# Kernel optimization log

Hardware: AMD Instinct MI355X
Metric: run time of the kernel (lower is better)

Reference implementation:

```python
import jax, jax.numpy as jnp
import numpy as np

D_MODEL = 1024
NUM_HEADS = 16
HEAD_DIM = D_MODEL // NUM_HEADS


def setup_inputs() -> dict:
    key = jax.random.key(0)
    ks = jax.random.split(key, 11)
    B, S = 2, 2048
    inp = {
        "query": jax.random.normal(ks[0], (B, S, D_MODEL), jnp.float32),
        "key": jax.random.normal(ks[1], (B, S, D_MODEL), jnp.float32),
        "value": jax.random.normal(ks[2], (B, S, D_MODEL), jnp.float32),
        "mask": 1,
        "w_q": jax.random.normal(ks[3], (D_MODEL, D_MODEL), jnp.float32) / np.sqrt(D_MODEL),
        "b_q": jax.random.normal(ks[4], (D_MODEL,), jnp.float32) * 0.02,
        "w_k": jax.random.normal(ks[5], (D_MODEL, D_MODEL), jnp.float32) / np.sqrt(D_MODEL),
        "b_k": jax.random.normal(ks[6], (D_MODEL,), jnp.float32) * 0.02,
        "w_v": jax.random.normal(ks[7], (D_MODEL, D_MODEL), jnp.float32) / np.sqrt(D_MODEL),
        "b_v": jax.random.normal(ks[8], (D_MODEL,), jnp.float32) * 0.02,
        "w_o": jax.random.normal(ks[9], (D_MODEL, D_MODEL), jnp.float32) / np.sqrt(D_MODEL),
        "b_o": jax.random.normal(ks[10], (D_MODEL,), jnp.float32) * 0.02,
    }
    return inp


def reference(query, key, value, mask, w_q, b_q, w_k, b_k, w_v, b_v, w_o, b_o):
    B, S, _ = query.shape
    H, Dh = NUM_HEADS, HEAD_DIM
    # projections (torch Linear: x @ W.T + b; here w_* stored as [in, out])
    q = (query @ w_q + b_q).reshape(B, S, H, Dh).transpose(0, 2, 1, 3)  # [B,H,S,Dh]
    k = (key @ w_k + b_k).reshape(B, S, H, Dh).transpose(0, 2, 1, 3)
    v = (value @ w_v + b_v).reshape(B, S, H, Dh).transpose(0, 2, 1, 3)
    scale = 1.0 / jnp.sqrt(jnp.asarray(Dh, q.dtype))
    scores = jnp.einsum("bhqd,bhkd->bhqk", q, k) * scale  # [B,H,S,S]
    if mask:
        causal = jnp.tril(jnp.ones((S, S), dtype=bool))
        scores = jnp.where(causal, scores, jnp.asarray(-1e9, scores.dtype))
    attn = jax.nn.softmax(scores, axis=-1)
    x = jnp.einsum("bhqk,bhkd->bhqd", attn, v)  # [B,H,S,Dh]
    x = x.transpose(0, 2, 1, 3).reshape(B, S, H * Dh)
    return x @ w_o + b_o
```

## Files before the change

kernel.cpp:

```cpp
#include <hip/hip_runtime.h>
#include <hip/hip_bf16.h>

using bf16 = __hip_bfloat16;

typedef __attribute__((ext_vector_type(4))) short short4v;
typedef __attribute__((ext_vector_type(8))) short short8v;
typedef __attribute__((ext_vector_type(4))) float f32x4;

static constexpr int D  = 1024;
static constexpr int H  = 16;
static constexpr int DH = 64;
static constexpr int B  = 2;
static constexpr int S  = 2048;
static constexpr int M  = B * S;
static constexpr size_t MD = (size_t)M * D;
static constexpr size_t WSZ = (size_t)D * D;

#define QS_CONST 0.18033688011112042f

__device__ __forceinline__ unsigned short f2b(float f) {
    union { float f; unsigned u; } v; v.f = f;
    return (unsigned short)((v.u + 0x7FFFu + ((v.u >> 16) & 1u)) >> 16);
}
__device__ __forceinline__ unsigned pkbf(float a, float b) {
    float2 t; t.x = a; t.y = b;
    __hip_bfloat162 h = __float22bfloat162_rn(t);
    union { __hip_bfloat162 h; unsigned u; } cv; cv.h = h;
    return cv.u;
}
__device__ __forceinline__ short8v pack8(short4v a, short4v b) {
    short8v r;
    r[0]=a[0]; r[1]=a[1]; r[2]=a[2]; r[3]=a[3];
    r[4]=b[0]; r[5]=b[1]; r[6]=b[2]; r[7]=b[3];
    return r;
}
__device__ __forceinline__ short8v ld_frag(const short* rowp, int lg) {
    short4v a = *reinterpret_cast<const short4v*>(rowp + 4*lg);
    short4v b = *reinterpret_cast<const short4v*>(rowp + 16 + 4*lg);
    return pack8(a, b);
}

__device__ __forceinline__ void gl_lds16(const void* g, void* l) {
    __builtin_amdgcn_global_load_lds(
        (const __attribute__((address_space(1))) unsigned int*)g,
        (__attribute__((address_space(3))) unsigned int*)l, 16, 0, 0);
}

__global__ __launch_bounds__(256) void cvt_x_kernel(
    const float* __restrict__ x0, const float* __restrict__ x1,
    const float* __restrict__ x2,
    unsigned short* __restrict__ y0, unsigned short* __restrict__ y1,
    unsigned short* __restrict__ y2)
{
    const float* X = blockIdx.z==0 ? x0 : blockIdx.z==1 ? x1 : x2;
    unsigned short* Y = blockIdx.z==0 ? y0 : blockIdx.z==1 ? y1 : y2;
    const size_t base = (size_t)blockIdx.x * 256 + threadIdx.x;
    const size_t stride = (size_t)1024 * 256;
#pragma unroll
    for (int j = 0; j < 4; ++j) {
        const size_t i = base + (size_t)j * stride;
        float4 f = reinterpret_cast<const float4*>(X)[i];
        uint2 p; p.x = pkbf(f.x, f.y); p.y = pkbf(f.z, f.w);
        reinterpret_cast<uint2*>(Y)[i] = p;
    }
}

__global__ __launch_bounds__(256) void cvt_w_kernel(
    const float* __restrict__ w0, const float* __restrict__ w1,
    const float* __restrict__ w2, const float* __restrict__ w3,
    unsigned short* __restrict__ t0, unsigned short* __restrict__ t1,
    unsigned short* __restrict__ t2, unsigned short* __restrict__ t3)
{
    __shared__ float tile[32][33];
    const float* W = blockIdx.z==0 ? w0 : blockIdx.z==1 ? w1 : blockIdx.z==2 ? w2 : w3;
    unsigned short* T = blockIdx.z==0 ? t0 : blockIdx.z==1 ? t1 : blockIdx.z==2 ? t2 : t3;
    const int k0 = blockIdx.x*32, n0 = blockIdx.y*32;
    const int t = threadIdx.x, r = t>>3, c4 = (t&7)*4;
    float4 v = *reinterpret_cast<const float4*>(&W[(size_t)(k0+r)*D + n0 + c4]);
    tile[r][c4+0]=v.x; tile[r][c4+1]=v.y; tile[r][c4+2]=v.z; tile[r][c4+3]=v.w;
    __syncthreads();
    uint2 p;
    p.x = pkbf(tile[c4+0][r], tile[c4+1][r]);
    p.y = pkbf(tile[c4+2][r], tile[c4+3][r]);
    *reinterpret_cast<uint2*>(T + (size_t)(n0+r)*D + k0 + c4) = p;
}

#define GEMM_CORE_LDS(XPTR, WPTR)                                              \
    __shared__ short As[2][128*32];                                            \
    __shared__ short Bs[2][128*32];                                            \
    const int tid = threadIdx.x;                                               \
    const int wid = tid>>6, lane = tid&63;                                     \
    const int wr = wid>>1, wc = wid&1;                                         \
    const int lg = lane>>4, lr = lane&15;                                      \
    const int qw = (lane&3) ^ ((lane>>3)&3);        \
    const int qr = lg ^ ((lr>>1)&3);                \
    f32x4 acc[4][4];                                                           \
    _Pragma("unroll")                                                          \
    for (int i=0;i<4;i++)                                                      \
        _Pragma("unroll")                                                      \
        for (int j=0;j<4;j++) acc[i][j] = f32x4{0.f,0.f,0.f,0.f};              \
    const int srow = (lane>>2);                                                \
    auto stage = [&](int buf, int k0) {                                        \
        _Pragma("unroll")                                                      \
        for (int c=0;c<2;c++) {                                                \
            const int r0 = 32*wid + 16*c;                                      \
            const int r  = r0 + srow;                                          \
            gl_lds16(XPTR + (size_t)(m0+r)*1024 + k0 + qw*8, &As[buf][r0*32]); \
            gl_lds16(WPTR + (size_t)(n0+r)*1024 + k0 + qw*8, &Bs[buf][r0*32]); \
        }                                                                      \
    };                                                                         \
    stage(0, 0);                                                               \
    int cur = 0;                                                               \
    for (int k0 = 0; k0 < 1024; k0 += 32) {                                    \
        __syncthreads();                     \
        if (k0 + 32 < 1024) stage(cur^1, k0 + 32);                             \
        short8v af[4], bfr[4];                                                 \
        _Pragma("unroll")                                                      \
        for (int i=0;i<4;i++) {                                                \
            const int R = wr*64 + i*16 + lr;                                   \
            af[i] = *reinterpret_cast<const short8v*>(&As[cur][R*32 + qr*8]);  \
        }                                                                      \
        _Pragma("unroll")                                                      \
        for (int j=0;j<4;j++) {                                                \
            const int R = wc*64 + j*16 + lr;                                   \
            bfr[j] = *reinterpret_cast<const short8v*>(&Bs[cur][R*32 + qr*8]); \
        }                                                                      \
        __builtin_amdgcn_s_setprio(1);                                         \
        _Pragma("unroll")                                                      \
        for (int i=0;i<4;i++)                                                  \
            _Pragma("unroll")                                                  \
            for (int j=0;j<4;j++)                                              \
                acc[i][j] = __builtin_amdgcn_mfma_f32_16x16x32_bf16(           \
                    af[i], bfr[j], acc[i][j], 0,0,0);                          \
        __builtin_amdgcn_s_setprio(0);                                         \
        cur ^= 1;                                                              \
    }

__global__ __launch_bounds__(256) void gemm_qkv_lds(
    const unsigned short* __restrict__ Xq, const unsigned short* __restrict__ Xk,
    const unsigned short* __restrict__ Xv, const unsigned short* __restrict__ WtBase,
    const float* __restrict__ bq, const float* __restrict__ bk,
    const float* __restrict__ bv, unsigned short* __restrict__ qkBase,
    unsigned short* __restrict__ va)
{
    const int z = blockIdx.z;
    const unsigned short* X = z==0 ? Xq : z==1 ? Xk : Xv;
    const unsigned short* Wt = WtBase + (size_t)z * WSZ;
    const float* bias = z==0 ? bq : z==1 ? bk : bv;
    const int m0 = blockIdx.x*128, n0 = blockIdx.y*128;

    GEMM_CORE_LDS(X, Wt)

#pragma unroll
    for (int i=0;i<4;i++) {
#pragma unroll
        for (int j=0;j<4;j++) {
            const int n = n0 + wc*64 + j*16 + lr;
            const float bv2 = bias[n];
#pragma unroll
            for (int r=0;r<4;r++) {
                const int m = m0 + wr*64 + i*16 + lg*4 + r;
                float v = acc[i][j][r] + bv2;
                const int bb=m>>11, ss=m&2047, hh=n>>6, dh=n&63;
                if (z == 0) {
                    v *= QS_CONST;
                    qkBase[(((size_t)(bb*H+hh))*S + ss)*DH + dh] = f2b(v);
                } else if (z == 1) {
                    (qkBase + MD)[(((size_t)(bb*H+hh))*S + ss)*DH + dh] = f2b(v);
                } else {
                    va[(((size_t)(bb*H+hh))*DH + dh)*S + ss] = f2b(v);
                }
            }
        }
    }
}

template<int OUTBF>
__global__ __launch_bounds__(256) void gemm_out_lds(
    const unsigned short* __restrict__ Xc, const unsigned short* __restrict__ Wt,
    const float* __restrict__ bias, void* __restrict__ Y)
{
    const int m0 = blockIdx.x*128, n0 = blockIdx.y*128;

    GEMM_CORE_LDS(Xc, Wt)

#pragma unroll
    for (int i=0;i<4;i++) {
#pragma unroll
        for (int j=0;j<4;j++) {
            const int n = n0 + wc*64 + j*16 + lr;
            const float bv = bias[n];
#pragma unroll
            for (int r=0;r<4;r++) {
                const int m = m0 + wr*64 + i*16 + lg*4 + r;
                const float v = acc[i][j][r] + bv;
                if (OUTBF) ((unsigned short*)Y)[(size_t)m*D + n] = f2b(v);
                else       ((float*)Y)[(size_t)m*D + n] = v;
            }
        }
    }
}

__global__ __launch_bounds__(256) void attn_mfma(
    const unsigned short* __restrict__ Qa,
    const unsigned short* __restrict__ Ka,
    const unsigned short* __restrict__ Va,
    unsigned short* __restrict__ Ctx)
{
    __shared__ short Ks[2][64][72];
    __shared__ short Vs[2][64][72];
    short (*Ob)[72] = Ks[0];

    const int tid = threadIdx.x;
    const int i   = blockIdx.x;
    const int xcd = i & 7;
    const int o   = i >> 3;
    const int bh  = (xcd << 2) + (o >> 5);
    const int qt  = ((o >> 5) & 1) ? (o & 31) : 31 - (o & 31);
    const int bb = bh>>4, hh = bh&15;
    const int q0 = qt*64;
    const int wid = tid>>6, lane = tid&63;
    const int lg = lane>>4, lr = lane&15;
    const size_t qkbase = (size_t)bh*S*DH;
    const size_t vbase  = (size_t)bh*DH*S;

    const int qrow = q0 + wid*16 + lr;
    short8v qf[2];
    {
        const unsigned short* qp = Qa + qkbase + (size_t)qrow*DH;
#pragma unroll
        for (int c=0;c<2;c++) {
            short4v a = *reinterpret_cast<const short4v*>(qp + 32*c + 4*lg);
            short4v b = *reinterpret_cast<const short4v*>(qp + 32*c + 16 + 4*lg);
            qf[c] = pack8(a, b);
        }
    }

    float lsum = 0.f;
    f32x4 oacc[4];
#pragma unroll
    for (int dt=0;dt<4;dt++) oacc[dt] = f32x4{0.f,0.f,0.f,0.f};

    const int sr = tid>>2;
    const int sc = (tid&3)*16;

    uint4 kg0, kg1, vg0, vg1;
    auto load_kv = [&](int j0) {
        const unsigned short* kp = Ka + qkbase + (size_t)(j0+sr)*DH + sc;
        kg0 = *reinterpret_cast<const uint4*>(kp);
        kg1 = *reinterpret_cast<const uint4*>(kp + 8);
        const unsigned short* vp = Va + vbase + (size_t)sr*S + j0 + sc;
        vg0 = *reinterpret_cast<const uint4*>(vp);
        vg1 = *reinterpret_cast<const uint4*>(vp + 8);
    };
    auto store_kv = [&](int buf) {
        *reinterpret_cast<uint4*>(&Ks[buf][sr][sc])   = kg0;
        *reinterpret_cast<uint4*>(&Ks[buf][sr][sc+8]) = kg1;
        *reinterpret_cast<uint4*>(&Vs[buf][sr][sc])   = vg0;
        *reinterpret_cast<uint4*>(&Vs[buf][sr][sc+8]) = vg1;
    };

    const int NT = qt + 1;
    load_kv(0);
    store_kv(0);

    for (int t = 0; t < NT; ++t) {
        const int j0 = t*64;
        const int cur = t & 1;
        if (t + 1 < NT) load_kv(j0 + 64);
        __syncthreads();

        __builtin_amdgcn_s_setprio(1);
        f32x4 st[4];
#pragma unroll
        for (int jt=0;jt<4;jt++) {
            f32x4 s = f32x4{0.f,0.f,0.f,0.f};
#pragma unroll
            for (int c=0;c<2;c++) {
                short8v kf = ld_frag(&Ks[cur][jt*16 + lr][32*c], lg);
                s = __builtin_amdgcn_mfma_f32_16x16x32_bf16(kf, qf[c], s, 0,0,0);
            }
            st[jt] = s;
        }
        __builtin_amdgcn_s_setprio(0);

        float p[16];
        if (t == NT-1) {
#pragma unroll
            for (int jt=0;jt<4;jt++)
#pragma unroll
                for (int r=0;r<4;r++) {
                    const int j = j0 + jt*16 + lg*4 + r;
                    p[jt*4+r] = (j <= qrow) ? st[jt][r] : -1e30f;
                }
        } else {
#pragma unroll
            for (int jt=0;jt<4;jt++)
#pragma unroll
                for (int r=0;r<4;r++) p[jt*4+r] = st[jt][r];
        }
#pragma unroll
        for (int e=0;e<16;e++) { p[e] = exp2f(p[e]); lsum += p[e]; }

        uint4 u0, u1;
        u0.x = pkbf(p[0],p[1]);   u0.y = pkbf(p[2],p[3]);
        u0.z = pkbf(p[4],p[5]);   u0.w = pkbf(p[6],p[7]);
        u1.x = pkbf(p[8],p[9]);   u1.y = pkbf(p[10],p[11]);
        u1.z = pkbf(p[12],p[13]); u1.w = pkbf(p[14],p[15]);
        short8v pf0, pf1;
        *reinterpret_cast<uint4*>(&pf0) = u0;
        *reinterpret_cast<uint4*>(&pf1) = u1;

        __builtin_amdgcn_s_setprio(1);
#pragma unroll
        for (int dt=0;dt<4;dt++) {
            short8v vf0 = ld_frag(&Vs[cur][dt*16 + lr][0],  lg);
            short8v vf1 = ld_frag(&Vs[cur][dt*16 + lr][32], lg);
            oacc[dt] = __builtin_amdgcn_mfma_f32_16x16x32_bf16(vf0, pf0, oacc[dt], 0,0,0);
            oacc[dt] = __builtin_amdgcn_mfma_f32_16x16x32_bf16(vf1, pf1, oacc[dt], 0,0,0);
        }
        __builtin_amdgcn_s_setprio(0);

        if (t + 1 < NT) store_kv(cur ^ 1);
    }

    lsum += __shfl_xor(lsum, 16);
    lsum += __shfl_xor(lsum, 32);
    __syncthreads();
    const float inv = 1.f / lsum;
#pragma unroll
    for (int dt=0;dt<4;dt++) {
        uint2 w;
        w.x = pkbf(oacc[dt][0]*inv, oacc[dt][1]*inv);
        w.y = pkbf(oacc[dt][2]*inv, oacc[dt][3]*inv);
        *reinterpret_cast<uint2*>(&Ob[wid*16 + lr][dt*16 + lg*4]) = w;
    }
    __syncthreads();
    const int orow = tid>>2, oc = (tid&3)*16;
    uint4 o1 = *reinterpret_cast<const uint4*>(&Ob[orow][oc]);
    uint4 o2 = *reinterpret_cast<const uint4*>(&Ob[orow][oc+8]);
    unsigned short* dst = Ctx + ((size_t)bb*S + q0 + orow)*D + hh*DH + oc;
    *reinterpret_cast<uint4*>(dst)     = o1;
    *reinterpret_cast<uint4*>(dst + 8) = o2;
}

__global__ __launch_bounds__(256) void gemm_qkv_f32(
    const float* __restrict__ Xq, const float* __restrict__ Xk,
    const float* __restrict__ Xv, const unsigned short* __restrict__ WtBase,
    const float* __restrict__ bq, const float* __restrict__ bk,
    const float* __restrict__ bv, unsigned short* __restrict__ qkBase,
    unsigned short* __restrict__ va)
{
    constexpr int K = 1024;
    __shared__ short As[128][40];
    __shared__ short Bs[128][40];

    const int z = blockIdx.z;
    const float* X = z==0 ? Xq : z==1 ? Xk : Xv;
    const unsigned short* Wt = WtBase + (size_t)z * WSZ;
    const float* bias = z==0 ? bq : z==1 ? bk : bv;

    const int tid = threadIdx.x;
    const int m0 = blockIdx.x*128, n0 = blockIdx.y*128;
    const int wid = tid>>6, lane = tid&63;
    const int wr = wid>>1, wc = wid&1;
    const int lg = lane>>4, lr = lane&15;

    f32x4 acc[4][4];
#pragma unroll
    for (int i=0;i<4;i++)
#pragma unroll
        for (int j=0;j<4;j++) acc[i][j] = f32x4{0.f,0.f,0.f,0.f};

    const int arow = tid>>1, acol = (tid&1)*16;
    float4 fx0, fx1, fx2, fx3;
    uint4 wa, wb;

    auto load_glb = [&](int k0) {
        const float* Xp = X + (size_t)(m0+arow)*K + k0 + acol;
        fx0 = *reinterpret_cast<const float4*>(Xp+0);
        fx1 = *reinterpret_cast<const float4*>(Xp+4);
        fx2 = *reinterpret_cast<const float4*>(Xp+8);
        fx3 = *reinterpret_cast<const float4*>(Xp+12);
        const unsigned short* Wp = Wt + (size_t)(n0+arow)*K + k0 + acol;
        wa = *reinterpret_cast<const uint4*>(Wp);
        wb = *reinterpret_cast<const uint4*>(Wp + 8);
    };
    auto store_stage = [&]() {
        uint4 p0; p0.x=pkbf(fx0.x,fx0.y); p0.y=pkbf(fx0.z,fx0.w);
                  p0.z=pkbf(fx1.x,fx1.y); p0.w=pkbf(fx1.z,fx1.w);
        uint4 p1; p1.x=pkbf(fx2.x,fx2.y); p1.y=pkbf(fx2.z,fx2.w);
                  p1.z=pkbf(fx3.x,fx3.y); p1.w=pkbf(fx3.z,fx3.w);
        *reinterpret_cast<uint4*>(&As[arow][acol])   = p0;
        *reinterpret_cast<uint4*>(&As[arow][acol+8]) = p1;
        *reinterpret_cast<uint4*>(&Bs[arow][acol])   = wa;
        *reinterpret_cast<uint4*>(&Bs[arow][acol+8]) = wb;
    };

    load_glb(0);
    for (int k0 = 0; k0 < K; k0 += 32) {
        __syncthreads();
        store_stage();
        if (k0 + 32 < K) load_glb(k0 + 32);
        __syncthreads();

        short8v af[4], bfr[4];
#pragma unroll
        for (int i=0;i<4;i++) af[i]  = ld_frag(&As[wr*64 + i*16 + lr][0], lg);
#pragma unroll
        for (int j=0;j<4;j++) bfr[j] = ld_frag(&Bs[wc*64 + j*16 + lr][0], lg);
#pragma unroll
        for (int i=0;i<4;i++)
#pragma unroll
            for (int j=0;j<4;j++)
                acc[i][j] = __builtin_amdgcn_mfma_f32_16x16x32_bf16(af[i], bfr[j], acc[i][j], 0,0,0);
    }

#pragma unroll
    for (int i=0;i<4;i++) {
#pragma unroll
        for (int j=0;j<4;j++) {
            const int n = n0 + wc*64 + j*16 + lr;
            const float bv2 = bias[n];
#pragma unroll
            for (int r=0;r<4;r++) {
                const int m = m0 + wr*64 + i*16 + lg*4 + r;
                float v = acc[i][j][r] + bv2;
                const int bb=m>>11, ss=m&2047, hh=n>>6, dh=n&63;
                if (z == 0) {
                    v *= QS_CONST;
                    qkBase[(((size_t)(bb*H+hh))*S + ss)*DH + dh] = f2b(v);
                } else if (z == 1) {
                    (qkBase + MD)[(((size_t)(bb*H+hh))*S + ss)*DH + dh] = f2b(v);
                } else {
                    va[(((size_t)(bb*H+hh))*DH + dh)*S + ss] = f2b(v);
                }
            }
        }
    }
}

extern "C" void kernel_launch(void* const* d_in, const int* in_sizes, int n_in,
                              void* d_out, int out_size, void* d_ws, size_t ws_size,
                              hipStream_t stream)
{
    const float* query = (const float*)d_in[0];
    const float* key   = (const float*)d_in[1];
    const float* value = (const float*)d_in[2];
    const float* w_q = (const float*)d_in[4];
    const float* b_q = (const float*)d_in[5];
    const float* w_k = (const float*)d_in[6];
    const float* b_k = (const float*)d_in[7];
    const float* w_v = (const float*)d_in[8];
    const float* b_v = (const float*)d_in[9];
    const float* w_o = (const float*)d_in[10];
    const float* b_o = (const float*)d_in[11];

    bool out_bf16 = true;
    {
        size_t ob = 0;
        if (hipMemPtrGetInfo(d_out, &ob) == hipSuccess &&
            ob >= (size_t)out_size * 3 && ob <= (size_t)out_size * 6)
            out_bf16 = false;
    }

    unsigned short* wtq = (unsigned short*)d_ws;
    unsigned short* wtk = wtq + WSZ;
    unsigned short* wtv = wtk + WSZ;
    unsigned short* wto = wtv + WSZ;
    unsigned short* qa  = wto + WSZ;
    unsigned short* ka  = qa  + MD;
    unsigned short* va  = ka  + MD;
    unsigned short* ctx = va  + MD;
    unsigned short* xq  = ctx + MD;
    unsigned short* xk  = xq  + MD;
    unsigned short* xv  = xk  + MD;

    const size_t need_bf16x = (4*WSZ + 7*MD) * sizeof(unsigned short);
    const bool xbf = (ws_size >= need_bf16x);

    cvt_w_kernel<<<dim3(32,32,4), 256, 0, stream>>>(w_q, w_k, w_v, w_o,
                                                    wtq, wtk, wtv, wto);

    if (xbf) {
        cvt_x_kernel<<<dim3(1024,1,3), 256, 0, stream>>>(query, key, value,
                                                         xq, xk, xv);
        gemm_qkv_lds<<<dim3(M/128, D/128, 3), 256, 0, stream>>>(
            xq, xk, xv, wtq, b_q, b_k, b_v, qa, va);
    } else {
        gemm_qkv_f32<<<dim3(M/128, D/128, 3), 256, 0, stream>>>(
            query, key, value, wtq, b_q, b_k, b_v, qa, va);
    }

    attn_mfma<<<dim3((S/64) * B * H), 256, 0, stream>>>(qa, ka, va, ctx);

    if (out_bf16)
        gemm_out_lds<1><<<dim3(M/128, D/128), 256, 0, stream>>>(ctx, wto, b_o, d_out);
    else
        gemm_out_lds<0><<<dim3(M/128, D/128), 256, 0, stream>>>(ctx, wto, b_o, d_out);
}
```

Baseline: 130.1 us.

## Merge conversion kernels and stage attention K/V via direct global-to-LDS loads

Merges the weight-transpose and activation-conversion kernels into one launch, which saves a launch and lets the two run concurrently. The attention kernel now copies K/V tiles with global_load_lds straight into XOR-swizzled unpadded LDS, issued right after the barrier for the next buffer. This replaces the register round-trip and the padding. The fp32 fallback GEMM path is removed, so the code now assumes the workspace is always large enough for the bf16 activations.

```diff
diff --git a/kernel.cpp b/kernel.cpp
--- a/kernel.cpp
+++ b/kernel.cpp
@@ -46,43 +46,43 @@
         (__attribute__((address_space(3))) unsigned int*)l, 16, 0, 0);
 }
 
-__global__ __launch_bounds__(256) void cvt_x_kernel(
+__global__ __launch_bounds__(256) void cvt_all_kernel(
+    const float* __restrict__ w0, const float* __restrict__ w1,
+    const float* __restrict__ w2, const float* __restrict__ w3,
+    unsigned short* __restrict__ t0, unsigned short* __restrict__ t1,
+    unsigned short* __restrict__ t2, unsigned short* __restrict__ t3,
     const float* __restrict__ x0, const float* __restrict__ x1,
     const float* __restrict__ x2,
     unsigned short* __restrict__ y0, unsigned short* __restrict__ y1,
     unsigned short* __restrict__ y2)
 {
-    const float* X = blockIdx.z==0 ? x0 : blockIdx.z==1 ? x1 : x2;
-    unsigned short* Y = blockIdx.z==0 ? y0 : blockIdx.z==1 ? y1 : y2;
-    const size_t base = (size_t)blockIdx.x * 256 + threadIdx.x;
-    const size_t stride = (size_t)1024 * 256;
-#pragma unroll
-    for (int j = 0; j < 4; ++j) {
-        const size_t i = base + (size_t)j * stride;
-        float4 f = reinterpret_cast<const float4*>(X)[i];
-        uint2 p; p.x = pkbf(f.x, f.y); p.y = pkbf(f.z, f.w);
-        reinterpret_cast<uint2*>(Y)[i] = p;
-    }
-}
-
-__global__ __launch_bounds__(256) void cvt_w_kernel(
-    const float* __restrict__ w0, const float* __restrict__ w1,
-    const float* __restrict__ w2, const float* __restrict__ w3,
-    unsigned short* __restrict__ t0, unsigned short* __restrict__ t1,
-    unsigned short* __restrict__ t2, unsigned short* __restrict__ t3)
-{
     __shared__ float tile[32][33];
-    const float* W = blockIdx.z==0 ? w0 : blockIdx.z==1 ? w1 : blockIdx.z==2 ? w2 : w3;
-    unsigned short* T = blockIdx.z==0 ? t0 : blockIdx.z==1 ? t1 : blockIdx.z==2 ? t2 : t3;
-    const int k0 = blockIdx.x*32, n0 = blockIdx.y*32;
-    const int t = threadIdx.x, r = t>>3, c4 = (t&7)*4;
-    float4 v = *reinterpret_cast<const float4*>(&W[(size_t)(k0+r)*D + n0 + c4]);
-    tile[r][c4+0]=v.x; tile[r][c4+1]=v.y; tile[r][c4+2]=v.z; tile[r][c4+3]=v.w;
-    __syncthreads();
-    uint2 p;
-    p.x = pkbf(tile[c4+0][r], tile[c4+1][r]);
-    p.y = pkbf(tile[c4+2][r], tile[c4+3][r]);
-    *reinterpret_cast<uint2*>(T + (size_t)(n0+r)*D + k0 + c4) = p;
+    const int z = blockIdx.z;
+    if (z < 4) {
+        const float* W = z==0 ? w0 : z==1 ? w1 : z==2 ? w2 : w3;
+        unsigned short* T = z==0 ? t0 : z==1 ? t1 : z==2 ? t2 : t3;
+        const int k0 = (blockIdx.x & 31) * 32, n0 = (blockIdx.x >> 5) * 32;
+        const int t = threadIdx.x, r = t>>3, c4 = (t&7)*4;
+        float4 v = *reinterpret_cast<const float4*>(&W[(size_t)(k0+r)*D + n0 + c4]);
+        tile[r][c4+0]=v.x; tile[r][c4+1]=v.y; tile[r][c4+2]=v.z; tile[r][c4+3]=v.w;
+        __syncthreads();
+        uint2 p;
+        p.x = pkbf(tile[c4+0][r], tile[c4+1][r]);
+        p.y = pkbf(tile[c4+2][r], tile[c4+3][r]);
+        *reinterpret_cast<uint2*>(T + (size_t)(n0+r)*D + k0 + c4) = p;
+    } else {
+        const float* X = z==4 ? x0 : z==5 ? x1 : x2;
+        unsigned short* Y = z==4 ? y0 : z==5 ? y1 : y2;
+        const size_t base = (size_t)blockIdx.x * 256 + threadIdx.x;
+        const size_t stride = (size_t)1024 * 256;
+#pragma unroll
+        for (int j = 0; j < 4; ++j) {
+            const size_t i = base + (size_t)j * stride;
+            float4 f = reinterpret_cast<const float4*>(X)[i];
+            uint2 p; p.x = pkbf(f.x, f.y); p.y = pkbf(f.z, f.w);
+            reinterpret_cast<uint2*>(Y)[i] = p;
+        }
+    }
 }
 
 #define GEMM_CORE_LDS(XPTR, WPTR)                                              \
@@ -207,9 +207,9 @@
     const unsigned short* __restrict__ Va,
     unsigned short* __restrict__ Ctx)
 {
-    __shared__ short Ks[2][64][72];
-    __shared__ short Vs[2][64][72];
-    short (*Ob)[72] = Ks[0];
+    __shared__ short Ks[2][64*64];
+    __shared__ short Vs[2][64*64];
+    short (*Ob)[72] = (short(*)[72])Ks;
 
     const int tid = threadIdx.x;
     const int i   = blockIdx.x;
@@ -241,34 +241,36 @@
 #pragma unroll
     for (int dt=0;dt<4;dt++) oacc[dt] = f32x4{0.f,0.f,0.f,0.f};
 
-    const int sr = tid>>2;
-    const int sc = (tid&3)*16;
-
-    uint4 kg0, kg1, vg0, vg1;
-    auto load_kv = [&](int j0) {
-        const unsigned short* kp = Ka + qkbase + (size_t)(j0+sr)*DH + sc;
-        kg0 = *reinterpret_cast<const uint4*>(kp);
-        kg1 = *reinterpret_cast<const uint4*>(kp + 8);
-        const unsigned short* vp = Va + vbase + (size_t)sr*S + j0 + sc;
-        vg0 = *reinterpret_cast<const uint4*>(vp);
-        vg1 = *reinterpret_cast<const uint4*>(vp + 8);
+    const int srsub = lane >> 3;
+    const int scol  = 8 * ((lane & 7) ^ srsub);
+
+    auto stage = [&](int buf, int j0) {
+#pragma unroll
+        for (int c2=0;c2<2;c2++) {
+            const int rb = 16*wid + 8*c2;
+            gl_lds16(Ka + qkbase + (size_t)(j0 + rb + srsub)*DH + scol,
+                     &Ks[buf][rb*64]);
+            gl_lds16(Va + vbase  + (size_t)(rb + srsub)*S + j0 + scol,
+                     &Vs[buf][rb*64]);
+        }
     };
-    auto store_kv = [&](int buf) {
-        *reinterpret_cast<uint4*>(&Ks[buf][sr][sc])   = kg0;
-        *reinterpret_cast<uint4*>(&Ks[buf][sr][sc+8]) = kg1;
-        *reinterpret_cast<uint4*>(&Vs[buf][sr][sc])   = vg0;
-        *reinterpret_cast<uint4*>(&Vs[buf][sr][sc+8]) = vg1;
-    };
+
+    const int r7 = lr & 7;
+    const int l4 = 4*(lg & 1), g0 = lg >> 1;
+    int offA[2], offB[2];
+#pragma unroll
+    for (int c=0;c<2;c++) {
+        offA[c] = l4 + 8*((4*c + g0)     ^ r7);
+        offB[c] = l4 + 8*((4*c + 2 + g0) ^ r7);
+    }
 
     const int NT = qt + 1;
-    load_kv(0);
-    store_kv(0);
-
+    stage(0, 0);
     for (int t = 0; t < NT; ++t) {
         const int j0 = t*64;
         const int cur = t & 1;
-        if (t + 1 < NT) load_kv(j0 + 64);
         __syncthreads();
+        if (t + 1 < NT) stage(cur ^ 1, j0 + 64);
 
         __builtin_amdgcn_s_setprio(1);
         f32x4 st[4];
@@ -277,8 +279,10 @@
             f32x4 s = f32x4{0.f,0.f,0.f,0.f};
 #pragma unroll
             for (int c=0;c<2;c++) {
-                short8v kf = ld_frag(&Ks[cur][jt*16 + lr][32*c], lg);
-                s = __builtin_amdgcn_mfma_f32_16x16x32_bf16(kf, qf[c], s, 0,0,0);
+                const short* rowp = &Ks[cur][(jt*16 + lr)*64];
+                short4v a = *reinterpret_cast<const short4v*>(rowp + offA[c]);
+                short4v b = *reinterpret_cast<const short4v*>(rowp + offB[c]);
+                s = __builtin_amdgcn_mfma_f32_16x16x32_bf16(pack8(a,b), qf[c], s, 0,0,0);
             }
             st[jt] = s;
         }
@@ -314,14 +318,15 @@
         __builtin_amdgcn_s_setprio(1);
 #pragma unroll
         for (int dt=0;dt<4;dt++) {
-            short8v vf0 = ld_frag(&Vs[cur][dt*16 + lr][0],  lg);
-            short8v vf1 = ld_frag(&Vs[cur][dt*16 + lr][32], lg);
-            oacc[dt] = __builtin_amdgcn_mfma_f32_16x16x32_bf16(vf0, pf0, oacc[dt], 0,0,0);
-            oacc[dt] = __builtin_amdgcn_mfma_f32_16x16x32_bf16(vf1, pf1, oacc[dt], 0,0,0);
+            const short* rowp = &Vs[cur][(dt*16 + lr)*64];
+            short4v a0 = *reinterpret_cast<const short4v*>(rowp + offA[0]);
+            short4v b0 = *reinterpret_cast<const short4v*>(rowp + offB[0]);
+            short4v a1 = *reinterpret_cast<const short4v*>(rowp + offA[1]);
+            short4v b1 = *reinterpret_cast<const short4v*>(rowp + offB[1]);
+            oacc[dt] = __builtin_amdgcn_mfma_f32_16x16x32_bf16(pack8(a0,b0), pf0, oacc[dt], 0,0,0);
+            oacc[dt] = __builtin_amdgcn_mfma_f32_16x16x32_bf16(pack8(a1,b1), pf1, oacc[dt], 0,0,0);
         }
         __builtin_amdgcn_s_setprio(0);
-
-        if (t + 1 < NT) store_kv(cur ^ 1);
     }
 
     lsum += __shfl_xor(lsum, 16);
@@ -342,102 +347,6 @@
     unsigned short* dst = Ctx + ((size_t)bb*S + q0 + orow)*D + hh*DH + oc;
     *reinterpret_cast<uint4*>(dst)     = o1;
     *reinterpret_cast<uint4*>(dst + 8) = o2;
-}
-
-__global__ __launch_bounds__(256) void gemm_qkv_f32(
-    const float* __restrict__ Xq, const float* __restrict__ Xk,
-    const float* __restrict__ Xv, const unsigned short* __restrict__ WtBase,
-    const float* __restrict__ bq, const float* __restrict__ bk,
-    const float* __restrict__ bv, unsigned short* __restrict__ qkBase,
-    unsigned short* __restrict__ va)
-{
-    constexpr int K = 1024;
-    __shared__ short As[128][40];
-    __shared__ short Bs[128][40];
-
-    const int z = blockIdx.z;
-    const float* X = z==0 ? Xq : z==1 ? Xk : Xv;
-    const unsigned short* Wt = WtBase + (size_t)z * WSZ;
-    const float* bias = z==0 ? bq : z==1 ? bk : bv;
-
-    const int tid = threadIdx.x;
-    const int m0 = blockIdx.x*128, n0 = blockIdx.y*128;
-    const int wid = tid>>6, lane = tid&63;
-    const int wr = wid>>1, wc = wid&1;
-    const int lg = lane>>4, lr = lane&15;
-
-    f32x4 acc[4][4];
-#pragma unroll
-    for (int i=0;i<4;i++)
-#pragma unroll
-        for (int j=0;j<4;j++) acc[i][j] = f32x4{0.f,0.f,0.f,0.f};
-
-    const int arow = tid>>1, acol = (tid&1)*16;
-    float4 fx0, fx1, fx2, fx3;
-    uint4 wa, wb;
-
-    auto load_glb = [&](int k0) {
-        const float* Xp = X + (size_t)(m0+arow)*K + k0 + acol;
-        fx0 = *reinterpret_cast<const float4*>(Xp+0);
-        fx1 = *reinterpret_cast<const float4*>(Xp+4);
-        fx2 = *reinterpret_cast<const float4*>(Xp+8);
-        fx3 = *reinterpret_cast<const float4*>(Xp+12);
-        const unsigned short* Wp = Wt + (size_t)(n0+arow)*K + k0 + acol;
-        wa = *reinterpret_cast<const uint4*>(Wp);
-        wb = *reinterpret_cast<const uint4*>(Wp + 8);
-    };
-    auto store_stage = [&]() {
-        uint4 p0; p0.x=pkbf(fx0.x,fx0.y); p0.y=pkbf(fx0.z,fx0.w);
-                  p0.z=pkbf(fx1.x,fx1.y); p0.w=pkbf(fx1.z,fx1.w);
-        uint4 p1; p1.x=pkbf(fx2.x,fx2.y); p1.y=pkbf(fx2.z,fx2.w);
-                  p1.z=pkbf(fx3.x,fx3.y); p1.w=pkbf(fx3.z,fx3.w);
-        *reinterpret_cast<uint4*>(&As[arow][acol])   = p0;
-        *reinterpret_cast<uint4*>(&As[arow][acol+8]) = p1;
-        *reinterpret_cast<uint4*>(&Bs[arow][acol])   = wa;
-        *reinterpret_cast<uint4*>(&Bs[arow][acol+8]) = wb;
-    };
-
-    load_glb(0);
-    for (int k0 = 0; k0 < K; k0 += 32) {
-        __syncthreads();
-        store_stage();
-        if (k0 + 32 < K) load_glb(k0 + 32);
-        __syncthreads();
-
-        short8v af[4], bfr[4];
-#pragma unroll
-        for (int i=0;i<4;i++) af[i]  = ld_frag(&As[wr*64 + i*16 + lr][0], lg);
-#pragma unroll
-        for (int j=0;j<4;j++) bfr[j] = ld_frag(&Bs[wc*64 + j*16 + lr][0], lg);
-#pragma unroll
-        for (int i=0;i<4;i++)
-#pragma unroll
-            for (int j=0;j<4;j++)
-                acc[i][j] = __builtin_amdgcn_mfma_f32_16x16x32_bf16(af[i], bfr[j], acc[i][j], 0,0,0);
-    }
-
-#pragma unroll
-    for (int i=0;i<4;i++) {
-#pragma unroll
-        for (int j=0;j<4;j++) {
-            const int n = n0 + wc*64 + j*16 + lr;
-            const float bv2 = bias[n];
-#pragma unroll
-            for (int r=0;r<4;r++) {
-                const int m = m0 + wr*64 + i*16 + lg*4 + r;
-                float v = acc[i][j][r] + bv2;
-                const int bb=m>>11, ss=m&2047, hh=n>>6, dh=n&63;
-                if (z == 0) {
-                    v *= QS_CONST;
-                    qkBase[(((size_t)(bb*H+hh))*S + ss)*DH + dh] = f2b(v);
-                } else if (z == 1) {
-                    (qkBase + MD)[(((size_t)(bb*H+hh))*S + ss)*DH + dh] = f2b(v);
-                } else {
-                    va[(((size_t)(bb*H+hh))*DH + dh)*S + ss] = f2b(v);
-                }
-            }
-        }
-    }
 }
 
 extern "C" void kernel_launch(void* const* d_in, const int* in_sizes, int n_in,
@@ -476,21 +385,12 @@
     unsigned short* xk  = xq  + MD;
     unsigned short* xv  = xk  + MD;
 
-    const size_t need_bf16x = (4*WSZ + 7*MD) * sizeof(unsigned short);
-    const bool xbf = (ws_size >= need_bf16x);
-
-    cvt_w_kernel<<<dim3(32,32,4), 256, 0, stream>>>(w_q, w_k, w_v, w_o,
-                                                    wtq, wtk, wtv, wto);
-
-    if (xbf) {
-        cvt_x_kernel<<<dim3(1024,1,3), 256, 0, stream>>>(query, key, value,
-                                                         xq, xk, xv);
-        gemm_qkv_lds<<<dim3(M/128, D/128, 3), 256, 0, stream>>>(
-            xq, xk, xv, wtq, b_q, b_k, b_v, qa, va);
-    } else {
-        gemm_qkv_f32<<<dim3(M/128, D/128, 3), 256, 0, stream>>>(
-            query, key, value, wtq, b_q, b_k, b_v, qa, va);
-    }
+    cvt_all_kernel<<<dim3(1024,1,7), 256, 0, stream>>>(
+        w_q, w_k, w_v, w_o, wtq, wtk, wtv, wto,
+        query, key, value, xq, xk, xv);
+
+    gemm_qkv_lds<<<dim3(M/128, D/128, 3), 256, 0, stream>>>(
+        xq, xk, xv, wtq, b_q, b_k, b_v, qa, va);
 
     attn_mfma<<<dim3((S/64) * B * H), 256, 0, stream>>>(qa, ka, va, ctx);
 
```

After: 134.6 us. +3.4%, slower.
